# Performance work log

Hardware: AMD Instinct MI355X
Metric: run time of the kernel (lower is better)

## Reference

```python
import jax, jax.numpy as jnp
import numpy as np
import math

D_EMB = 1024
N_HEADS = 16
D_HEAD = D_EMB // N_HEADS
D_FF = 4 * D_EMB
BATCH = 2
SEQ = 2048
EPS = 1e-6


def setup_inputs() -> dict:
    key = jax.random.key(0)
    ks = jax.random.split(key, 12)
    s = 0.02
    return {
        "x": jax.random.normal(ks[0], (BATCH, SEQ, D_EMB), jnp.float32),
        "wq": jax.random.normal(ks[1], (D_EMB, D_EMB), jnp.float32) * s,
        "wk": jax.random.normal(ks[2], (D_EMB, D_EMB), jnp.float32) * s,
        "wv": jax.random.normal(ks[3], (D_EMB, D_EMB), jnp.float32) * s,
        "wo": jax.random.normal(ks[4], (D_EMB, D_EMB), jnp.float32) * s,
        "bo": jnp.zeros((D_EMB,), jnp.float32),
        "w1": jax.random.normal(ks[5], (D_FF, D_EMB), jnp.float32) * s,
        "b1": jnp.zeros((D_FF,), jnp.float32),
        "w2": jax.random.normal(ks[6], (D_EMB, D_FF), jnp.float32) * s,
        "b2": jnp.zeros((D_EMB,), jnp.float32),
        "ln1_s": jnp.ones((D_EMB,), jnp.float32),
        "ln1_b": jnp.zeros((D_EMB,), jnp.float32),
        "ln2_s": jnp.ones((D_EMB,), jnp.float32),
        "ln2_b": jnp.zeros((D_EMB,), jnp.float32),
    }


def _layernorm(x, scale, shift):
    mean = jnp.mean(x, axis=-1, keepdims=True)
    var = jnp.mean(jnp.square(x - mean), axis=-1, keepdims=True)  # unbiased=False
    return scale * (x - mean) / jnp.sqrt(var + EPS) + shift


def _gelu_tanh(x):
    c = math.sqrt(2.0 / math.pi)
    return 0.5 * x * (1.0 + jnp.tanh(c * (x + 0.044715 * x * x * x)))


def _attention(x, wq, wk, wv, wo, bo):
    B, S, _ = x.shape
    q = (x @ wq.T).reshape(B, S, N_HEADS, D_HEAD).transpose(0, 2, 1, 3)
    k = (x @ wk.T).reshape(B, S, N_HEADS, D_HEAD).transpose(0, 2, 1, 3)
    v = (x @ wv.T).reshape(B, S, N_HEADS, D_HEAD).transpose(0, 2, 1, 3)
    scores = jnp.einsum("bhqd,bhkd->bhqk", q, k)
    causal = jnp.triu(jnp.ones((S, S), bool), k=1)
    scores = jnp.where(causal, -jnp.inf, scores)
    weights = jax.nn.softmax(scores / math.sqrt(D_HEAD), axis=-1)
    ctx = jnp.einsum("bhqk,bhkd->bhqd", weights, v)
    ctx = ctx.transpose(0, 2, 1, 3).reshape(B, S, D_EMB)
    return ctx @ wo.T + bo


def reference(x, wq, wk, wv, wo, bo, w1, b1, w2, b2, ln1_s, ln1_b, ln2_s, ln2_b):
    # pre-norm attention block (dropout in eval mode = identity)
    h = x + _attention(_layernorm(x, ln1_s, ln1_b), wq, wk, wv, wo, bo)
    # pre-norm MLP with tanh-approx GeLU
    y = _layernorm(h, ln2_s, ln2_b)
    y = _gelu_tanh(y @ w1.T + b1) @ w2.T + b2
    return h + y
```

## Files before the change

kernel.cpp:

```cpp
#include <hip/hip_runtime.h>
#include <math.h>

typedef unsigned short u16;
typedef __attribute__((ext_vector_type(8))) __bf16 bf16x8v;
typedef __attribute__((ext_vector_type(8))) unsigned short ushort8v;
typedef __attribute__((ext_vector_type(4))) unsigned short ushort4v;
typedef __attribute__((ext_vector_type(4))) float f32x4v;

#define D_EMBD 1024
#define NHEADS 16
#define DHEAD  64
#define DFF    4096
#define BATCHN 2
#define SEQL   2048
#define TOK    (BATCHN*SEQL)

#define EPI_BF16_GELU    2
#define EPI_BF16_QKV     3
#define EPI_BF16_PART    5

__device__ __forceinline__ float bf2f(u16 s) {
  return __builtin_bit_cast(float, (unsigned)s << 16);
}
__device__ __forceinline__ u16 f2bf(float f) {
  unsigned u = __builtin_bit_cast(unsigned, f);
  unsigned r = u + 0x7fffu + ((u >> 16) & 1u);
  return (u16)(r >> 16);
}
__device__ __forceinline__ u16 f2bf_trunc(float f) {
  return (u16)(__builtin_bit_cast(unsigned, f) >> 16);
}

#define GLOAD16(gp, lp)                                                        \
  __builtin_amdgcn_global_load_lds(                                            \
      (__attribute__((address_space(1))) void*)(void*)(gp),                    \
      (__attribute__((address_space(3))) void*)(void*)(lp), 16, 0, 0)

__global__ __launch_bounds__(256) void prep_kernel(const float* __restrict__ wq,
                                                   const float* __restrict__ wk,
                                                   const float* __restrict__ wv,
                                                   const float* __restrict__ wo,
                                                   const float* __restrict__ w1,
                                                   const float* __restrict__ w2,
                                                   u16* __restrict__ wcat,
                                                   u16* __restrict__ wob,
                                                   u16* __restrict__ w1b,
                                                   u16* __restrict__ w2b,
                                                   const float* __restrict__ x,
                                                   const float* __restrict__ sc,
                                                   const float* __restrict__ sh,
                                                   u16* __restrict__ xn) {
  int bid = blockIdx.x, tid = threadIdx.x;
  if (bid < 12288) {
    const float* src;
    u16* dst;
    int loc;
    if (bid < 4096) {
      int seg = bid >> 10;
      loc = (bid & 1023) * 256 + tid;
      src = (seg == 0) ? wq : (seg == 1) ? wk : (seg == 2) ? wv : wo;
      dst = (seg == 0) ? wcat : (seg == 1) ? wcat + 1048576
                              : (seg == 2) ? wcat + 2097152 : wob;
    } else if (bid < 8192) {
      loc = (bid - 4096) * 256 + tid;
      src = w1; dst = w1b;
    } else {
      loc = (bid - 8192) * 256 + tid;
      src = w2; dst = w2b;
    }
    float4 v = ((const float4*)src)[loc];
    ushort4 o;
    o.x = f2bf(v.x); o.y = f2bf(v.y); o.z = f2bf(v.z); o.w = f2bf(v.w);
    ((ushort4*)dst)[loc] = o;
    return;
  }
  int row = bid - 12288;
  const float4* xr = (const float4*)(x + (size_t)row * D_EMBD);
  float4 v = xr[tid];
  float s  = (v.x + v.y) + (v.z + v.w);
  float s2 = (v.x * v.x + v.y * v.y) + (v.z * v.z + v.w * v.w);
#pragma unroll
  for (int off = 32; off; off >>= 1) {
    s  += __shfl_xor(s, off, 64);
    s2 += __shfl_xor(s2, off, 64);
  }
  __shared__ float rs[4], rs2[4];
  int wave = tid >> 6, lane = tid & 63;
  if (lane == 0) { rs[wave] = s; rs2[wave] = s2; }
  __syncthreads();
  s  = (rs[0] + rs[1]) + (rs[2] + rs[3]);
  s2 = (rs2[0] + rs2[1]) + (rs2[2] + rs2[3]);
  float mean = s * (1.f / 1024.f);
  float var  = s2 * (1.f / 1024.f) - mean * mean;
  float rstd = rsqrtf(var + 1e-6f);
  float4 scv = ((const float4*)sc)[tid];
  float4 shv = ((const float4*)sh)[tid];
  ushort4 o;
  o.x = f2bf((v.x - mean) * rstd * scv.x + shv.x);
  o.y = f2bf((v.y - mean) * rstd * scv.y + shv.y);
  o.z = f2bf((v.z - mean) * rstd * scv.z + shv.z);
  o.w = f2bf((v.w - mean) * rstd * scv.w + shv.w);
  ((ushort4*)(xn + (size_t)row * D_EMBD))[tid] = o;
}

__global__ __launch_bounds__(256) void ln2f_kernel(const u16* __restrict__ parts,
                                                   const float* __restrict__ x,
                                                   const float* __restrict__ bo,
                                                   const float* __restrict__ sc,
                                                   const float* __restrict__ sh,
                                                   float* __restrict__ hbuf,
                                                   u16* __restrict__ ybuf) {
  int row = blockIdx.x, tid = threadIdx.x;
  size_t base4 = (size_t)row * 256 + tid;
  float4 v = ((const float4*)x)[base4];
  float4 bv = ((const float4*)bo)[tid];
  v.x += bv.x; v.y += bv.y; v.z += bv.z; v.w += bv.w;
#pragma unroll
  for (int p = 0; p < 4; ++p) {
    ushort4 u = ((const ushort4*)parts)[(size_t)p * 1048576 + base4];
    v.x += bf2f(u.x); v.y += bf2f(u.y); v.z += bf2f(u.z); v.w += bf2f(u.w);
  }
  ((float4*)hbuf)[base4] = v;
  float s  = (v.x + v.y) + (v.z + v.w);
  float s2 = (v.x * v.x + v.y * v.y) + (v.z * v.z + v.w * v.w);
#pragma unroll
  for (int off = 32; off; off >>= 1) {
    s  += __shfl_xor(s, off, 64);
    s2 += __shfl_xor(s2, off, 64);
  }
  __shared__ float rs[4], rs2[4];
  int wave = tid >> 6, lane = tid & 63;
  if (lane == 0) { rs[wave] = s; rs2[wave] = s2; }
  __syncthreads();
  s  = (rs[0] + rs[1]) + (rs[2] + rs[3]);
  s2 = (rs2[0] + rs2[1]) + (rs2[2] + rs2[3]);
  float mean = s * (1.f / 1024.f);
  float var  = s2 * (1.f / 1024.f) - mean * mean;
  float rstd = rsqrtf(var + 1e-6f);
  float4 scv = ((const float4*)sc)[tid];
  float4 shv = ((const float4*)sh)[tid];
  ushort4 o;
  o.x = f2bf((v.x - mean) * rstd * scv.x + shv.x);
  o.y = f2bf((v.y - mean) * rstd * scv.y + shv.y);
  o.z = f2bf((v.z - mean) * rstd * scv.z + shv.z);
  o.w = f2bf((v.w - mean) * rstd * scv.w + shv.w);
  ((ushort4*)ybuf)[base4] = o;
}

__global__ __launch_bounds__(256) void reduce_w2_kernel(const u16* __restrict__ parts,
                                                        const float* __restrict__ resid,
                                                        const float* __restrict__ bias,
                                                        float* __restrict__ out) {
  int i = blockIdx.x * 256 + threadIdx.x;
  float4 r = ((const float4*)resid)[i];
  float4 bi = ((const float4*)bias)[i & 255];
  float s0 = 0, s1 = 0, s2 = 0, s3 = 0;
#pragma unroll
  for (int p = 0; p < 4; ++p) {
    ushort4 u = ((const ushort4*)parts)[(size_t)p * 1048576 + i];
    s0 += bf2f(u.x); s1 += bf2f(u.y); s2 += bf2f(u.z); s3 += bf2f(u.w);
  }
  float4 o = {s0 + r.x + bi.x, s1 + r.y + bi.y, s2 + r.z + bi.z, s3 + r.w + bi.w};
  ((float4*)out)[i] = o;
}

#define GBAR  __builtin_amdgcn_s_barrier()
#define LGKM0 do { asm volatile("s_waitcnt lgkmcnt(0)" ::: "memory"); \
                   __builtin_amdgcn_sched_barrier(0); } while (0)

template <int EPI>
__global__ __launch_bounds__(512, 2) void gemm256(const u16* __restrict__ A,
                                                  const u16* __restrict__ W,
                                                  u16* __restrict__ Cb,
                                                  const float* __restrict__ bias,
                                                  int M, int N, int K) {
  __shared__ __align__(16) u16 sm[65536];
  const int tid = threadIdx.x;
  const int wave = tid >> 6, lane = tid & 63;
  const int lr = lane & 15, quad = lane >> 4;
  const int wm = wave >> 2, wn = wave & 3;
  const int gx = gridDim.x, gy = gridDim.y;
  const int nwg = gx * gy * gridDim.z;
  const int bid = blockIdx.x + gx * (blockIdx.y + gy * blockIdx.z);
  const int swz = (bid & 7) * (nwg >> 3) + (bid >> 3);
  const int bx = swz % gx;
  const int r1 = swz / gx;
  const int by = r1 % gy, bz = r1 / gy;
  const int m0 = by * 256, n0 = bx * 256;
  const int KC = K / gridDim.z;
  const int kbeg = bz * KC;
  const int NT = KC >> 6;
  const size_t poff = (size_t)bz * ((size_t)M * N);

  const int r8 = lane >> 3;
  const int sslot = (lane & 7) ^ r8;
  const int rb0 = wave * 2;
  const int sx = lr & 7;

  auto stA = [&](int bb, int h, int tk) {
#pragma unroll
    for (int s = 0; s < 2; ++s) {
      const u16* gp = A + (size_t)(m0 + h * 128 + (rb0 + s) * 8 + r8) * K +
                      (kbeg + tk * 64 + sslot * 8);
      GLOAD16(gp, (char*)sm + bb * 65536 + h * 16384 + (rb0 + s) * 1024);
    }
  };
  auto stB = [&](int bb, int h, int tk) {
#pragma unroll
    for (int s = 0; s < 2; ++s) {
      const u16* gp = W + (size_t)(n0 + h * 128 + (rb0 + s) * 8 + r8) * K +
                      (kbeg + tk * 64 + sslot * 8);
      GLOAD16(gp, (char*)sm + bb * 65536 + 32768 + h * 16384 + (rb0 + s) * 1024);
    }
  };
  auto ldA = [&](bf16x8v (&av)[4][2], int mh, int cur) {
#pragma unroll
    for (int j2 = 0; j2 < 4; ++j2) {
      int row = (2 * (mh * 4 + j2) + wm) * 16 + lr;
#pragma unroll
      for (int kk = 0; kk < 2; ++kk) {
        int slot = (kk * 4 + quad) ^ sx;
        av[j2][kk] = *(const bf16x8v*)(sm + cur * 32768 + row * 64 + slot * 8);
      }
    }
  };
  auto ldB = [&](bf16x8v (&bv)[2][2], int nh, int cur) {
#pragma unroll
    for (int i2 = 0; i2 < 2; ++i2) {
      int row = (wn + 4 * (nh * 2 + i2)) * 16 + lr;
#pragma unroll
      for (int kk = 0; kk < 2; ++kk) {
        int slot = (kk * 4 + quad) ^ sx;
        bv[i2][kk] = *(const bf16x8v*)(sm + cur * 32768 + 16384 + row * 64 + slot * 8);
      }
    }
  };

  f32x4v acc[8][4];
#pragma unroll
  for (int j = 0; j < 8; ++j)
#pragma unroll
    for (int i = 0; i < 4; ++i) {
      f32x4v z = {0.f, 0.f, 0.f, 0.f};
      acc[j][i] = z;
    }
  bf16x8v av[4][2], bv0[2][2], bv1[2][2];

  auto MMA32 = [&](int mh) {
    GBAR;
    LGKM0;
    __builtin_amdgcn_s_setprio(1);
#pragma unroll
    for (int j2 = 0; j2 < 4; ++j2)
#pragma unroll
      for (int i2 = 0; i2 < 2; ++i2)
#pragma unroll
        for (int kk = 0; kk < 2; ++kk) {
          acc[mh * 4 + j2][i2] = __builtin_amdgcn_mfma_f32_16x16x32_bf16(
              av[j2][kk], bv0[i2][kk], acc[mh * 4 + j2][i2], 0, 0, 0);
          acc[mh * 4 + j2][2 + i2] = __builtin_amdgcn_mfma_f32_16x16x32_bf16(
              av[j2][kk], bv1[i2][kk], acc[mh * 4 + j2][2 + i2], 0, 0, 0);
        }
    __builtin_amdgcn_s_setprio(0);
    __builtin_amdgcn_sched_barrier(0);
    GBAR;
  };

  stA(0, 0, 0); stB(0, 0, 0); stA(0, 1, 0); stB(0, 1, 0);
  stA(1, 0, 1); stB(1, 1, 1);
  asm volatile("s_waitcnt vmcnt(4)" ::: "memory");
  GBAR;

  for (int t = 0; t < NT; ++t) {
    const int cur = t & 1, nb = cur ^ 1;
    const bool p1 = (t + 1 < NT), p2 = (t + 2 < NT);
    ldA(av, 0, cur); ldB(bv0, 0, cur); ldB(bv1, 1, cur);
    if (p1) { stB(nb, 0, t + 1); stA(nb, 1, t + 1); }
    MMA32(0);
    ldA(av, 1, cur);
    if (p2) { stA(cur, 0, t + 2); stB(cur, 1, t + 2); }
    if (p2) { asm volatile("s_waitcnt vmcnt(4)" ::: "memory"); }
    else    { asm volatile("s_waitcnt vmcnt(0)" ::: "memory"); }
    MMA32(1);
  }

  const bool qsc = (EPI == EPI_BF16_QKV) && (n0 < 1024);
#pragma unroll
  for (int j = 0; j < 8; ++j) {
    int gr = m0 + (2 * j + wm) * 16 + quad * 4;
#pragma unroll
    for (int i = 0; i < 4; ++i) {
      int gc = n0 + (wn + 4 * i) * 16 + lr;
      float bi = 0.f;
      if constexpr (EPI == EPI_BF16_GELU) bi = bias[gc];
#pragma unroll
      for (int r = 0; r < 4; ++r) {
        size_t idx = (size_t)(gr + r) * N + gc;
        float v = acc[j][i][r];
        if constexpr (EPI == EPI_BF16_PART) {
          Cb[poff + idx] = f2bf(v);
        } else if constexpr (EPI == EPI_BF16_QKV) {
          Cb[idx] = f2bf(qsc ? v * 0.18033688011112042f : v);
        } else {
          v += bi;
          float z = 0.7978845608028654f * (v + 0.044715f * v * v * v);
          float tt = 2.f / (1.f + __expf(-2.f * z)) - 1.f;
          Cb[idx] = f2bf(0.5f * v * (1.f + tt));
        }
      }
    }
  }
}

#define VTS 72
__device__ __forceinline__ void stage_k(const u16* Kbase, int ks, u16* kfbuf,
                                        int wave, int lr, int quad) {
#pragma unroll
  for (int p = 0; p < 2; ++p) {
    int q = wave * 2 + p;
    int key = ((q >> 1) << 4) + lr;
    int c8 = ((q & 1) << 2) + quad;
    GLOAD16(Kbase + (size_t)(ks + key) * 3072 + c8 * 8, (char*)kfbuf + q * 1024);
  }
}
__device__ __forceinline__ void load_v(const u16* Vbase, int ks, int vkey0, int vc8,
                                       ushort8v& va, ushort8v& vb) {
  va = *(const ushort8v*)(Vbase + (size_t)(ks + vkey0) * 3072 + vc8 * 8);
  vb = *(const ushort8v*)(Vbase + (size_t)(ks + vkey0 + 1) * 3072 + vc8 * 8);
}
__device__ __forceinline__ void write_vt(u16* vt, int vc8, int vcol,
                                         ushort8v va, ushort8v vb) {
#pragma unroll
  for (int j = 0; j < 8; ++j) {
    unsigned pk = (unsigned)va[j] | ((unsigned)vb[j] << 16);
    *(unsigned*)(vt + (size_t)(vc8 * 8 + j) * VTS + vcol) = pk;
  }
}

__global__ __launch_bounds__(256) void attn_kernel(const u16* __restrict__ qkv,
                                                   u16* __restrict__ ctx) {
  __shared__ u16 Kf[2][4096];
  __shared__ u16 Vt[2][64 * VTS];
  int tid = threadIdx.x;
  int wave = tid >> 6, lane = tid & 63;
  int lr = lane & 15, quad = lane >> 4;
  int id = blockIdx.x;
  int bh = id & 31;
  int t = 31 - (id >> 5);
  int b = bh >> 4, h = bh & 15;
  int q0 = t * 64;
  const u16* qkvb = qkv + (size_t)(b * SEQL) * 3072;
  int qrow = q0 + wave * 16 + lr;
  const u16* Qp = qkvb + (size_t)qrow * 3072 + h * 64 + quad * 8;
  bf16x8v qf0 = *(const bf16x8v*)(Qp);
  bf16x8v qf1 = *(const bf16x8v*)(Qp + 32);
  const u16* Kbase = qkvb + 1024 + h * 64;
  const u16* Vbase = qkvb + 2048 + h * 64;
  int vkey0 = (tid >> 3) * 2, vc8 = tid & 7;
  int vcol = vkey0 ^ (vc8 << 2);

  float m = -INFINITY, l = 0.f;
  f32x4v accO[4];
#pragma unroll
  for (int r = 0; r < 4; r++) {
    f32x4v z = {0.f, 0.f, 0.f, 0.f};
    accO[r] = z;
  }

  int nkt = t + 1;
  {
    stage_k(Kbase, 0, Kf[0], wave, lr, quad);
    ushort8v va, vb;
    load_v(Vbase, 0, vkey0, vc8, va, vb);
    write_vt(Vt[0], vc8, vcol, va, vb);
  }
  __syncthreads();

  for (int kt = 0; kt < nkt; ++kt) {
    int cur = kt & 1, nxt = cur ^ 1;
    ushort8v va, vb;
    bool pre = (kt + 1 < nkt);
    if (pre) {
      stage_k(Kbase, (kt + 1) * 64, Kf[nxt], wave, lr, quad);
      load_v(Vbase, (kt + 1) * 64, vkey0, vc8, va, vb);
    }
    const bf16x8v* Kc = (const bf16x8v*)Kf[cur];
    const u16* Vc = Vt[cur];
    f32x4v accS[4];
#pragma unroll
    for (int jb = 0; jb < 4; jb++) {
      f32x4v z = {0.f, 0.f, 0.f, 0.f};
      accS[jb] = z;
    }
#pragma unroll
    for (int jb = 0; jb < 4; jb++) {
      accS[jb] = __builtin_amdgcn_mfma_f32_16x16x32_bf16(Kc[((jb * 2 + 0) << 6) + lane], qf0, accS[jb], 0, 0, 0);
      accS[jb] = __builtin_amdgcn_mfma_f32_16x16x32_bf16(Kc[((jb * 2 + 1) << 6) + lane], qf1, accS[jb], 0, 0, 0);
    }
    if (kt == t) {
#pragma unroll
      for (int jb = 0; jb < 4; jb++)
#pragma unroll
        for (int r = 0; r < 4; r++)
          if (jb * 16 + quad * 4 + r > wave * 16 + lr) accS[jb][r] = -INFINITY;
    }
    float smax = accS[0][0];
#pragma unroll
    for (int jb = 0; jb < 4; jb++)
#pragma unroll
      for (int r = 0; r < 4; r++) smax = fmaxf(smax, accS[jb][r]);
    smax = fmaxf(smax, __shfl_xor(smax, 16, 64));
    smax = fmaxf(smax, __shfl_xor(smax, 32, 64));
    if (!__all(smax <= m + 8.f)) {
      float mn = fmaxf(m, smax);
      float alpha = __builtin_amdgcn_exp2f(m - mn);
      m = mn;
      l *= alpha;
      float ar[4];
#pragma unroll
      for (int r = 0; r < 4; r++) ar[r] = __shfl(alpha, quad * 4 + r, 16);
#pragma unroll
      for (int nb = 0; nb < 4; nb++)
#pragma unroll
        for (int r = 0; r < 4; r++) accO[nb][r] *= ar[r];
    }
    float ps = 0.f;
#pragma unroll
    for (int jb = 0; jb < 4; jb++)
#pragma unroll
      for (int r = 0; r < 4; r++) {
        accS[jb][r] = __builtin_amdgcn_exp2f(accS[jb][r] - m);
        ps += accS[jb][r];
      }
    ps += __shfl_xor(ps, 16, 64);
    ps += __shfl_xor(ps, 32, 64);
    l += ps;
#pragma unroll
    for (int kk = 0; kk < 2; ++kk) {
      ushort8v pp;
#pragma unroll
      for (int j = 0; j < 4; ++j) {
        pp[j]     = f2bf_trunc(accS[2 * kk][j]);
        pp[j + 4] = f2bf_trunc(accS[2 * kk + 1][j]);
      }
      bf16x8v pav = __builtin_bit_cast(bf16x8v, pp);
#pragma unroll
      for (int nb = 0; nb < 4; nb++) {
        int dim = nb * 16 + lr;
        int f = (nb * 2 + (lr >> 3)) & 7;
        int col1 = (kk * 32 + quad * 4) ^ (f << 2);
        ushort4v v0 = *(const ushort4v*)(Vc + dim * VTS + col1);
        ushort4v v1 = *(const ushort4v*)(Vc + dim * VTS + (col1 ^ 16));
        ushort8v vv;
#pragma unroll
        for (int j = 0; j < 4; ++j) { vv[j] = v0[j]; vv[j + 4] = v1[j]; }
        accO[nb] = __builtin_amdgcn_mfma_f32_16x16x32_bf16(pav, __builtin_bit_cast(bf16x8v, vv), accO[nb], 0, 0, 0);
      }
    }
    if (pre) write_vt(Vt[nxt], vc8, vcol, va, vb);
    __syncthreads();
  }
  float linv = 1.f / l;
  float rr[4];
#pragma unroll
  for (int r = 0; r < 4; r++) rr[r] = __shfl(linv, quad * 4 + r, 16);
#pragma unroll
  for (int nb = 0; nb < 4; nb++)
#pragma unroll
    for (int r = 0; r < 4; r++) {
      int rowg = q0 + wave * 16 + quad * 4 + r;
      ctx[(size_t)(b * SEQL + rowg) * D_EMBD + h * 64 + nb * 16 + lr] =
          f2bf(accO[nb][r] * rr[r]);
    }
}

extern "C" void kernel_launch(void* const* d_in, const int* in_sizes, int n_in,
                              void* d_out, int out_size, void* d_ws, size_t ws_size,
                              hipStream_t stream) {
  const float* x    = (const float*)d_in[0];
  const float* wq   = (const float*)d_in[1];
  const float* wk   = (const float*)d_in[2];
  const float* wv   = (const float*)d_in[3];
  const float* wo   = (const float*)d_in[4];
  const float* bo   = (const float*)d_in[5];
  const float* w1   = (const float*)d_in[6];
  const float* b1   = (const float*)d_in[7];
  const float* w2   = (const float*)d_in[8];
  const float* b2   = (const float*)d_in[9];
  const float* ln1s = (const float*)d_in[10];
  const float* ln1b = (const float*)d_in[11];
  const float* ln2s = (const float*)d_in[12];
  const float* ln2b = (const float*)d_in[13];
  float* out = (float*)d_out;

  char* base = (char*)d_ws;
  size_t off = 0;
  auto alloc = [&](size_t bytes) {
    char* r = base + off;
    off += (bytes + 255) & ~(size_t)255;
    return r;
  };
  u16*   wcat = (u16*)alloc((size_t)3072 * 1024 * 2);
  u16*   wob  = (u16*)alloc((size_t)1024 * 1024 * 2);
  u16*   w1b  = (u16*)alloc((size_t)4096 * 1024 * 2);
  u16*   w2b  = (u16*)alloc((size_t)1024 * 4096 * 2);
  u16*   xn   = (u16*)alloc((size_t)TOK * 1024 * 2);
  u16*   qkv  = (u16*)alloc((size_t)TOK * 3072 * 2);
  u16*   ctx  = (u16*)alloc((size_t)TOK * 1024 * 2);
  float* hbuf = (float*)alloc((size_t)TOK * 1024 * 4);
  u16*   ybuf = (u16*)alloc((size_t)TOK * 1024 * 2);
  u16*   gbuf = (u16*)alloc((size_t)TOK * 4096 * 2);
  u16* woP = (u16*)xn;
  u16* w2P = (u16*)xn;

  prep_kernel<<<16384, 256, 0, stream>>>(wq, wk, wv, wo, w1, w2,
                                         wcat, wob, w1b, w2b,
                                         x, ln1s, ln1b, xn);
  gemm256<EPI_BF16_QKV><<<dim3(12, 16), 512, 0, stream>>>(
      xn, wcat, qkv, nullptr, TOK, 3072, 1024);
  attn_kernel<<<1024, 256, 0, stream>>>(qkv, ctx);
  gemm256<EPI_BF16_PART><<<dim3(4, 16, 4), 512, 0, stream>>>(
      ctx, wob, woP, nullptr, TOK, 1024, 1024);
  ln2f_kernel<<<TOK, 256, 0, stream>>>(woP, x, bo, ln2s, ln2b, hbuf, ybuf);
  gemm256<EPI_BF16_GELU><<<dim3(16, 16), 512, 0, stream>>>(
      ybuf, w1b, gbuf, b1, TOK, 4096, 1024);
  gemm256<EPI_BF16_PART><<<dim3(4, 16, 4), 512, 0, stream>>>(
      gbuf, w2b, w2P, nullptr, TOK, 1024, 4096);
  reduce_w2_kernel<<<4096, 256, 0, stream>>>(w2P, hbuf, b2, out);
}
```

Baseline: 325.4 us.

## Use 256x192 tiles for QKV GEMM to fill all compute units

Result: no change. 325.6 us (+0.1%).

```diff
diff --git a/kernel.cpp b/kernel.cpp
--- a/kernel.cpp
+++ b/kernel.cpp
@@ -168,7 +168,7 @@
 #define LGKM0 do { asm volatile("s_waitcnt lgkmcnt(0)" ::: "memory"); \
                    __builtin_amdgcn_sched_barrier(0); } while (0)
 
-template <int EPI>
+template <int EPI, int NF = 4>
 __global__ __launch_bounds__(512, 2) void gemm256(const u16* __restrict__ A,
                                                   const u16* __restrict__ W,
                                                   u16* __restrict__ Cb,
@@ -186,7 +186,7 @@
   const int bx = swz % gx;
   const int r1 = swz / gx;
   const int by = r1 % gy, bz = r1 / gy;
-  const int m0 = by * 256, n0 = bx * 256;
+  const int m0 = by * 256, n0 = bx * (NF * 64);
   const int KC = K / gridDim.z;
   const int kbeg = bz * KC;
   const int NT = KC >> 6;
@@ -213,6 +213,11 @@
       GLOAD16(gp, (char*)sm + bb * 65536 + 32768 + h * 16384 + (rb0 + s) * 1024);
     }
   };
+  auto stBch = [&](int bb, int ch, int tk) {
+    const u16* gp = W + (size_t)(n0 + ch * 64 + wave * 8 + r8) * K +
+                    (kbeg + tk * 64 + sslot * 8);
+    GLOAD16(gp, (char*)sm + bb * 65536 + 32768 + ch * 8192 + wave * 1024);
+  };
   auto ldA = [&](bf16x8v (&av)[4][2], int mh, int cur) {
 #pragma unroll
     for (int j2 = 0; j2 < 4; ++j2) {
@@ -224,14 +229,14 @@
       }
     }
   };
-  auto ldB = [&](bf16x8v (&bv)[2][2], int nh, int cur) {
-#pragma unroll
-    for (int i2 = 0; i2 < 2; ++i2) {
-      int row = (wn + 4 * (nh * 2 + i2)) * 16 + lr;
+  auto ldB = [&](bf16x8v (&bv)[4][2], int cur) {
+#pragma unroll
+    for (int ii = 0; ii < NF; ++ii) {
+      int row = (wn + 4 * ii) * 16 + lr;
 #pragma unroll
       for (int kk = 0; kk < 2; ++kk) {
         int slot = (kk * 4 + quad) ^ sx;
-        bv[i2][kk] = *(const bf16x8v*)(sm + cur * 32768 + 16384 + row * 64 + slot * 8);
+        bv[ii][kk] = *(const bf16x8v*)(sm + cur * 32768 + 16384 + row * 64 + slot * 8);
       }
     }
   };
@@ -244,7 +249,7 @@
       f32x4v z = {0.f, 0.f, 0.f, 0.f};
       acc[j][i] = z;
     }
-  bf16x8v av[4][2], bv0[2][2], bv1[2][2];
+  bf16x8v av[4][2], bv[4][2];
 
   auto MMA32 = [&](int mh) {
     GBAR;
@@ -253,46 +258,64 @@
 #pragma unroll
     for (int j2 = 0; j2 < 4; ++j2)
 #pragma unroll
-      for (int i2 = 0; i2 < 2; ++i2)
-#pragma unroll
-        for (int kk = 0; kk < 2; ++kk) {
-          acc[mh * 4 + j2][i2] = __builtin_amdgcn_mfma_f32_16x16x32_bf16(
-              av[j2][kk], bv0[i2][kk], acc[mh * 4 + j2][i2], 0, 0, 0);
-          acc[mh * 4 + j2][2 + i2] = __builtin_amdgcn_mfma_f32_16x16x32_bf16(
-              av[j2][kk], bv1[i2][kk], acc[mh * 4 + j2][2 + i2], 0, 0, 0);
-        }
+      for (int ii = 0; ii < NF; ++ii)
+#pragma unroll
+        for (int kk = 0; kk < 2; ++kk)
+          acc[mh * 4 + j2][ii] = __builtin_amdgcn_mfma_f32_16x16x32_bf16(
+              av[j2][kk], bv[ii][kk], acc[mh * 4 + j2][ii], 0, 0, 0);
     __builtin_amdgcn_s_setprio(0);
     __builtin_amdgcn_sched_barrier(0);
     GBAR;
   };
 
-  stA(0, 0, 0); stB(0, 0, 0); stA(0, 1, 0); stB(0, 1, 0);
-  stA(1, 0, 1); stB(1, 1, 1);
-  asm volatile("s_waitcnt vmcnt(4)" ::: "memory");
+  if constexpr (NF == 4) {
+    stA(0, 0, 0); stB(0, 0, 0); stA(0, 1, 0); stB(0, 1, 0);
+    stA(1, 0, 1); stB(1, 1, 1);
+    asm volatile("s_waitcnt vmcnt(4)" ::: "memory");
+  } else {
+    stA(0, 0, 0); stBch(0, 0, 0); stBch(0, 1, 0); stBch(0, 2, 0); stA(0, 1, 0);
+    if (NT > 1) {
+      stA(1, 0, 1);
+      asm volatile("s_waitcnt vmcnt(2)" ::: "memory");
+    } else {
+      asm volatile("s_waitcnt vmcnt(0)" ::: "memory");
+    }
+  }
   GBAR;
 
   for (int t = 0; t < NT; ++t) {
     const int cur = t & 1, nb = cur ^ 1;
     const bool p1 = (t + 1 < NT), p2 = (t + 2 < NT);
-    ldA(av, 0, cur); ldB(bv0, 0, cur); ldB(bv1, 1, cur);
-    if (p1) { stB(nb, 0, t + 1); stA(nb, 1, t + 1); }
+    ldA(av, 0, cur); ldB(bv, cur);
+    if constexpr (NF == 4) {
+      if (p1) { stB(nb, 0, t + 1); stA(nb, 1, t + 1); }
+    } else {
+      if (p1) { stBch(nb, 0, t + 1); stBch(nb, 1, t + 1); stBch(nb, 2, t + 1);
+                stA(nb, 1, t + 1); }
+    }
     MMA32(0);
     ldA(av, 1, cur);
-    if (p2) { stA(cur, 0, t + 2); stB(cur, 1, t + 2); }
-    if (p2) { asm volatile("s_waitcnt vmcnt(4)" ::: "memory"); }
-    else    { asm volatile("s_waitcnt vmcnt(0)" ::: "memory"); }
+    if constexpr (NF == 4) {
+      if (p2) { stA(cur, 0, t + 2); stB(cur, 1, t + 2); }
+      if (p2) { asm volatile("s_waitcnt vmcnt(4)" ::: "memory"); }
+      else    { asm volatile("s_waitcnt vmcnt(0)" ::: "memory"); }
+    } else {
+      if (p2) { stA(cur, 0, t + 2); }
+      if (p2) { asm volatile("s_waitcnt vmcnt(2)" ::: "memory"); }
+      else    { asm volatile("s_waitcnt vmcnt(0)" ::: "memory"); }
+    }
     MMA32(1);
   }
 
-  const bool qsc = (EPI == EPI_BF16_QKV) && (n0 < 1024);
 #pragma unroll
   for (int j = 0; j < 8; ++j) {
     int gr = m0 + (2 * j + wm) * 16 + quad * 4;
 #pragma unroll
-    for (int i = 0; i < 4; ++i) {
+    for (int i = 0; i < NF; ++i) {
       int gc = n0 + (wn + 4 * i) * 16 + lr;
       float bi = 0.f;
       if constexpr (EPI == EPI_BF16_GELU) bi = bias[gc];
+      const bool qsc = (EPI == EPI_BF16_QKV) && (n0 + (wn + 4 * i) * 16 < 1024);
 #pragma unroll
       for (int r = 0; r < 4; ++r) {
         size_t idx = (size_t)(gr + r) * N + gc;
@@ -516,7 +539,7 @@
   prep_kernel<<<16384, 256, 0, stream>>>(wq, wk, wv, wo, w1, w2,
                                          wcat, wob, w1b, w2b,
                                          x, ln1s, ln1b, xn);
-  gemm256<EPI_BF16_QKV><<<dim3(12, 16), 512, 0, stream>>>(
+  gemm256<EPI_BF16_QKV, 3><<<dim3(16, 16), 512, 0, stream>>>(
       xn, wcat, qkv, nullptr, TOK, 3072, 1024);
   attn_kernel<<<1024, 256, 0, stream>>>(qkv, ctx);
   gemm256<EPI_BF16_PART><<<dim3(4, 16, 4), 512, 0, stream>>>(
```
